# Performance work log

Measured on AMD Instinct MI355X. Metric: run time of the kernel, lower is better.

## Reference

```python
import jax, jax.numpy as jnp
import numpy as np


def setup_inputs() -> dict:
    key = jax.random.key(0)
    k1, k2, k3, k4, k5 = jax.random.split(key, 5)
    N, M, K = 200000, 50, 4
    T = 1000.0
    ti = jnp.sort(jax.random.uniform(k1, (N,), dtype=jnp.float32) * T)
    mi = jax.random.randint(k2, (N,), 0, M, dtype=jnp.int64)
    mu_at_events = jax.random.uniform(k3, (N,), dtype=jnp.float32) * 0.5 + 0.05
    alpha = jax.random.uniform(k4, (K, M, M), dtype=jnp.float32) * 0.1
    gamma = jax.random.uniform(k5, (K,), dtype=jnp.float32) * 2.0 + 0.5
    return {"ti": ti, "mi": mi, "mu_at_events": mu_at_events, "alpha": alpha, "gamma": gamma}


def _hawkes_logsum(ti, mi, mu_at_events, alpha, gamma):
    # ti: [N] sorted event times; mi: [N] event types in [0, M)
    # alpha: [K, M, M]; gamma: [K]; mu_at_events: [N]
    N = ti.shape[0]
    M = alpha.shape[1]
    # inter-event gaps; dt[0] = 0 so the first event has zero excitation state
    dt = jnp.concatenate([jnp.zeros((1,), ti.dtype), ti[1:] - ti[:-1]])  # [N]
    a = jnp.exp(-gamma[None, :] * dt[:, None])  # [N, K] decay factors
    # one-hot of the PREVIOUS event's type (row 0 is all-zero, matching e_mi)
    prev_onehot = jnp.zeros((N, M), ti.dtype).at[jnp.arange(1, N), mi[:-1]].set(1.0)
    b = a[:, None, :] * prev_onehot[:, :, None]  # [N, M, K]

    # linear recurrence S_i = a_i * S_{i-1} + b_i via associative scan
    # combine((a1,b1),(a2,b2)) = (a1*a2, a2*b1 + b2)
    def combine(x, y):
        a1, b1 = x
        a2, b2 = y
        return (a1 * a2, a2[:, None, :] * b1 + b2)

    _, S = jax.lax.associative_scan(combine, (a, b))  # S: [N, M, K]
    # S[i, m, k] = sum_{j < i, m_j = m} exp(-gamma_k (t_i - t_j))
    alpha_at = alpha[:, mi, :]  # [K, N, M] rows of alpha for each event's type
    lam = mu_at_events + jnp.einsum('knm,nmk,k->n', alpha_at, S, gamma)  # [N]
    return jnp.sum(jnp.log(lam))


def reference(ti, mi, mu_at_events, alpha, gamma):
    return _hawkes_logsum(ti, mi, mu_at_events, alpha, gamma)
```

## Files before the change

kernel.cpp:

```cpp
#include <hip/hip_runtime.h>
#include <hip/hip_bf16.h>

#define CHUNK 256
#define MM 50
#define KK 4
#define STATE (MM*KK)
#define ASTRIDE 51
#define SUP 32
#define NSMAX 26
#define NSUB 8
#define SUBSZ 32

__device__ __forceinline__ unsigned short f2bf(float x) {
  unsigned u = __float_as_uint(x);
  u += 0x7fffu + ((u >> 16) & 1u);
  return (unsigned short)(u >> 16);
}

__global__ __launch_bounds__(256) void phase1(
    const float* __restrict__ ti, const int* __restrict__ mi,
    const float* __restrict__ gamma, float* __restrict__ chunkB,
    float* __restrict__ superB, float* __restrict__ out0, int N, int G) {
  int g = blockIdx.x, tid = threadIdx.x;
  if (g == 0 && tid == 0) out0[0] = 0.f;
  int l = g * CHUNK;
  int r = min(N, l + CHUNK);
  __shared__ float Bs[STATE];
  __shared__ float g4[KK];
  if (tid < STATE) Bs[tid] = 0.f;
  if (tid < KK) g4[tid] = gamma[tid];
  __syncthreads();
  float t_end = ti[r - 1];
  int j0 = (g == 0) ? 0 : (l - 1);
  int j = j0 + tid;
  if (j <= r - 2) {
    int m = mi[j];
    float dt = t_end - ti[j];
    #pragma unroll
    for (int k = 0; k < KK; ++k)
      atomicAdd(&Bs[m * KK + k], __expf(-g4[k] * dt));
  }
  __syncthreads();
  if (tid < STATE) {
    float v = Bs[tid];
    chunkB[(size_t)g * STATE + tid] = v;
    int sup = g / SUP;
    float gk = g4[tid & 3];
    float Tsup = ti[min(N, (sup + 1) * SUP * CHUNK) - 1];
    atomicAdd(&superB[(size_t)sup * STATE + tid], __expf(-gk * (Tsup - t_end)) * v);
  }
}

__global__ __launch_bounds__(512) void phase3(
    const float* __restrict__ ti, const int* __restrict__ mi,
    const float* __restrict__ mu, const float* __restrict__ alpha,
    const float* __restrict__ gamma, const float* __restrict__ chunkB,
    const float* __restrict__ superB, float* __restrict__ out, int N, int G) {
  int g = blockIdx.x, tid = threadIdx.x;
  int l = g * CHUNK;
  int r = min(N, l + CHUNK);
  int cnt = r - l;
  int sup = g / SUP;
  int g0 = sup * SUP;
  int e = tid >> 1;
  int h = tid & 1;

  __shared__ unsigned P0[MM * ASTRIDE];
  __shared__ unsigned P1[MM * ASTRIDE];
  __shared__ __align__(16) float4 Fj[CHUNK];
  __shared__ int   cj[CHUNK];
  __shared__ __align__(16) float Q[NSUB][STATE];
  __shared__ float red8[8];
  __shared__ float teL[SUP];
  __shared__ float tlast[NSMAX];

  float gk0 = gamma[0], gk1 = gamma[1], gk2 = gamma[2], gk3 = gamma[3];

  for (int i = tid; i < NSUB * STATE; i += 512) ((float*)Q)[i] = 0.f;

  for (int idx = tid; idx < MM * MM; idx += 512) {
    int c = idx / MM, cp = idx - c * MM;
    float a0 = gk0 * alpha[idx];
    float a1 = gk1 * alpha[2500 + idx];
    float a2 = gk2 * alpha[5000 + idx];
    float a3 = gk3 * alpha[7500 + idx];
    P0[c * ASTRIDE + cp] = (unsigned)f2bf(a0) | ((unsigned)f2bf(a1) << 16);
    P1[c * ASTRIDE + cp] = (unsigned)f2bf(a2) | ((unsigned)f2bf(a3) << 16);
  }

  if (tid < SUP) {
    int c = g0 + tid;
    if (c < G) teL[tid] = ti[min(N, (c + 1) * CHUNK) - 1];
  } else if (tid >= 64 && tid < 64 + NSMAX) {
    int s = tid - 64;
    if (s < sup) tlast[s] = ti[min(N, (s + 1) * SUP * CHUNK) - 1];
  }

  float t_ref = ti[(g == 0) ? 0 : (l - 1)];
  if (tid < CHUNK) {
    int j = l - 1 + tid;
    bool valid = (j >= 0) && (j <= r - 2);
    float4 myF = make_float4(0.f, 0.f, 0.f, 0.f);
    int myc = 0;
    if (valid) {
      myc = mi[j];
      float tj = ti[j] - t_ref;
      myF = make_float4(__expf(gk0 * tj), __expf(gk1 * tj),
                        __expf(gk2 * tj), __expf(gk3 * tj));
    }
    cj[tid] = myc;
    Fj[tid] = myF;
    __syncthreads();
    if (valid) {
      float* q = &Q[tid >> 5][myc * KK];
      atomicAdd(q + 0, myF.x); atomicAdd(q + 1, myF.y);
      atomicAdd(q + 2, myF.z); atomicAdd(q + 3, myF.w);
    }
  } else {
    __syncthreads();
  }

  float S = 0.f;
  if (tid < STATE) {
    float gk = gamma[tid & 3];
    int nloc = g - g0;
    #pragma unroll 4
    for (int u = 0; u < nloc; ++u)
      S += __expf(-gk * (t_ref - teL[u])) * chunkB[(size_t)(g0 + u) * STATE + tid];
    #pragma unroll 4
    for (int s = 0; s < sup; ++s)
      S += __expf(-gk * (t_ref - tlast[s])) * superB[(size_t)s * STATE + tid];
  }
  __syncthreads();

  if (tid < STATE) {
    float run = S;
    #pragma unroll
    for (int q = 0; q < NSUB; ++q) {
      float t = Q[q][tid];
      Q[q][tid] = run;
      run += t;
    }
  }
  __syncthreads();

  float local = 0.f;
  {
    int c_n = (e < cnt) ? mi[l + e] : 0;
    int rowb = c_n * ASTRIDE;
    const float4* wb = (const float4*)&Q[e >> 5][0];
    float4 acc = make_float4(0.f, 0.f, 0.f, 0.f);
    if (e < cnt) {
      int mlo = h * 25, mhi = mlo + 25;
      #pragma unroll 5
      for (int m = mlo; m < mhi; ++m) {
        unsigned p0 = P0[rowb + m];
        unsigned p1 = P1[rowb + m];
        float4 w = wb[m];
        acc.x += __uint_as_float(p0 << 16)         * w.x;
        acc.y += __uint_as_float(p0 & 0xffff0000u) * w.y;
        acc.z += __uint_as_float(p1 << 16)         * w.z;
        acc.w += __uint_as_float(p1 & 0xffff0000u) * w.w;
      }
      #pragma unroll 4
      for (int s = (e & ~(SUBSZ - 1)) + h; s <= e; s += 2) {
        unsigned p0 = P0[rowb + cj[s]];
        unsigned p1 = P1[rowb + cj[s]];
        float4 f = Fj[s];
        acc.x += __uint_as_float(p0 << 16)         * f.x;
        acc.y += __uint_as_float(p0 & 0xffff0000u) * f.y;
        acc.z += __uint_as_float(p1 << 16)         * f.z;
        acc.w += __uint_as_float(p1 & 0xffff0000u) * f.w;
      }
    }
    acc.x += __shfl_xor(acc.x, 1, 64);
    acc.y += __shfl_xor(acc.y, 1, 64);
    acc.z += __shfl_xor(acc.z, 1, 64);
    acc.w += __shfl_xor(acc.w, 1, 64);
    if (h == 0 && e < cnt) {
      float tn = ti[l + e] - t_ref;
      float lam = mu[l + e]
                + __expf(-gk0 * tn) * acc.x + __expf(-gk1 * tn) * acc.y
                + __expf(-gk2 * tn) * acc.z + __expf(-gk3 * tn) * acc.w;
      local = __logf(lam);
    }
  }
  #pragma unroll
  for (int off = 32; off > 0; off >>= 1)
    local += __shfl_down(local, off, 64);
  if ((tid & 63) == 0) red8[tid >> 6] = local;
  __syncthreads();
  if (tid == 0) {
    float t = 0.f;
    #pragma unroll
    for (int w = 0; w < 8; ++w) t += red8[w];
    atomicAdd(out, t);
  }
}

extern "C" void kernel_launch(void* const* d_in, const int* in_sizes, int n_in,
                              void* d_out, int out_size, void* d_ws, size_t ws_size,
                              hipStream_t stream) {
  const float* ti    = (const float*)d_in[0];
  const int*   mi    = (const int*)d_in[1];
  const float* mu    = (const float*)d_in[2];
  const float* alpha = (const float*)d_in[3];
  const float* gamma = (const float*)d_in[4];
  float* out = (float*)d_out;
  int N = in_sizes[0];
  int G = (N + CHUNK - 1) / CHUNK;

  float* superB = (float*)d_ws;
  float* chunkB = superB + (size_t)NSMAX * STATE;

  phase1<<<G, 256, 0, stream>>>(ti, mi, gamma, chunkB, superB, out, N, G);
  phase3<<<G, 512, 0, stream>>>(ti, mi, mu, alpha, gamma, chunkB, superB, out, N, G);
}
```

Measured before the change: 89.60 us.

## Fuse both phases into one decoupled-lookback kernel with ticket-ordered chunks

Merges the chunk-summary pass and the evaluation pass into a single kernel. Each block takes a dynamic ticket for its chunk, computes its chunk summary from the already-built Q sums, and publishes it through flag variables in global memory. Later blocks spin-wait on earlier chunk flags and on superchunk flags before evaluating. This removes one kernel launch and the duplicate reads of ti and mi, at the cost of serialised spin-waits across blocks and a dependence on an epoch counter kept in persistent device globals.

Result: slower. 191.0 us (+113.2%).

```diff
diff --git a/kernel.cpp b/kernel.cpp
--- a/kernel.cpp
+++ b/kernel.cpp
@@ -1,5 +1,4 @@
 #include <hip/hip_runtime.h>
-#include <hip/hip_bf16.h>
 
 #define CHUNK 256
 #define MM 50
@@ -10,6 +9,13 @@
 #define NSMAX 26
 #define NSUB 8
 #define SUBSZ 32
+#define GMAX 1024
+
+__device__ int      g_ticket;
+__device__ unsigned g_flag[GMAX];
+__device__ unsigned g_sflag[64];
+__device__ float    g_chunkB[GMAX * STATE];
+__device__ float    g_superB[64 * STATE];
 
 __device__ __forceinline__ unsigned short f2bf(float x) {
   unsigned u = __float_as_uint(x);
@@ -17,54 +23,12 @@
   return (unsigned short)(u >> 16);
 }
 
-__global__ __launch_bounds__(256) void phase1(
-    const float* __restrict__ ti, const int* __restrict__ mi,
-    const float* __restrict__ gamma, float* __restrict__ chunkB,
-    float* __restrict__ superB, float* __restrict__ out0, int N, int G) {
-  int g = blockIdx.x, tid = threadIdx.x;
-  if (g == 0 && tid == 0) out0[0] = 0.f;
-  int l = g * CHUNK;
-  int r = min(N, l + CHUNK);
-  __shared__ float Bs[STATE];
-  __shared__ float g4[KK];
-  if (tid < STATE) Bs[tid] = 0.f;
-  if (tid < KK) g4[tid] = gamma[tid];
-  __syncthreads();
-  float t_end = ti[r - 1];
-  int j0 = (g == 0) ? 0 : (l - 1);
-  int j = j0 + tid;
-  if (j <= r - 2) {
-    int m = mi[j];
-    float dt = t_end - ti[j];
-    #pragma unroll
-    for (int k = 0; k < KK; ++k)
-      atomicAdd(&Bs[m * KK + k], __expf(-g4[k] * dt));
-  }
-  __syncthreads();
-  if (tid < STATE) {
-    float v = Bs[tid];
-    chunkB[(size_t)g * STATE + tid] = v;
-    int sup = g / SUP;
-    float gk = g4[tid & 3];
-    float Tsup = ti[min(N, (sup + 1) * SUP * CHUNK) - 1];
-    atomicAdd(&superB[(size_t)sup * STATE + tid], __expf(-gk * (Tsup - t_end)) * v);
-  }
-}
-
-__global__ __launch_bounds__(512) void phase3(
+__global__ __launch_bounds__(512) void hawkes_fused(
     const float* __restrict__ ti, const int* __restrict__ mi,
     const float* __restrict__ mu, const float* __restrict__ alpha,
-    const float* __restrict__ gamma, const float* __restrict__ chunkB,
-    const float* __restrict__ superB, float* __restrict__ out, int N, int G) {
-  int g = blockIdx.x, tid = threadIdx.x;
-  int l = g * CHUNK;
-  int r = min(N, l + CHUNK);
-  int cnt = r - l;
-  int sup = g / SUP;
-  int g0 = sup * SUP;
-  int e = tid >> 1;
-  int h = tid & 1;
-
+    const float* __restrict__ gamma, float* __restrict__ out, int N, int G) {
+  int tid = threadIdx.x;
+  __shared__ int vid_s;
   __shared__ unsigned P0[MM * ASTRIDE];
   __shared__ unsigned P1[MM * ASTRIDE];
   __shared__ __align__(16) float4 Fj[CHUNK];
@@ -74,6 +38,8 @@
   __shared__ float teL[SUP];
   __shared__ float tlast[NSMAX];
 
+  if (tid == 0) vid_s = atomicAdd(&g_ticket, 1);
+
   float gk0 = gamma[0], gk1 = gamma[1], gk2 = gamma[2], gk3 = gamma[3];
 
   for (int i = tid; i < NSUB * STATE; i += 512) ((float*)Q)[i] = 0.f;
@@ -87,6 +53,19 @@
     P0[c * ASTRIDE + cp] = (unsigned)f2bf(a0) | ((unsigned)f2bf(a1) << 16);
     P1[c * ASTRIDE + cp] = (unsigned)f2bf(a2) | ((unsigned)f2bf(a3) << 16);
   }
+  __syncthreads();
+
+  int tkt = vid_s;
+  int epoch = tkt / G;
+  int g = tkt - epoch * G;
+  unsigned DONE = (unsigned)epoch + 1u;
+  int l = g * CHUNK;
+  int r = min(N, l + CHUNK);
+  int cnt = r - l;
+  int sup = g / SUP;
+  int g0 = sup * SUP;
+  int e = tid >> 1;
+  int h = tid & 1;
 
   if (tid < SUP) {
     int c = g0 + tid;
@@ -97,11 +76,12 @@
   }
 
   float t_ref = ti[(g == 0) ? 0 : (l - 1)];
+  bool valid = false;
+  int myc = 0;
+  float4 myF = make_float4(0.f, 0.f, 0.f, 0.f);
   if (tid < CHUNK) {
     int j = l - 1 + tid;
-    bool valid = (j >= 0) && (j <= r - 2);
-    float4 myF = make_float4(0.f, 0.f, 0.f, 0.f);
-    int myc = 0;
+    valid = (j >= 0) && (j <= r - 2);
     if (valid) {
       myc = mi[j];
       float tj = ti[j] - t_ref;
@@ -110,36 +90,78 @@
     }
     cj[tid] = myc;
     Fj[tid] = myF;
-    __syncthreads();
-    if (valid) {
-      float* q = &Q[tid >> 5][myc * KK];
-      atomicAdd(q + 0, myF.x); atomicAdd(q + 1, myF.y);
-      atomicAdd(q + 2, myF.z); atomicAdd(q + 3, myF.w);
-    }
-  } else {
-    __syncthreads();
-  }
+  }
+  __syncthreads();
+
+  if (valid) {
+    float* q = &Q[tid >> 5][myc * KK];
+    atomicAdd(q + 0, myF.x); atomicAdd(q + 1, myF.y);
+    atomicAdd(q + 2, myF.z); atomicAdd(q + 3, myF.w);
+  }
+  __syncthreads();
+
+  float gk = (tid & 2) ? ((tid & 1) ? gk3 : gk2) : ((tid & 1) ? gk1 : gk0);
+  float Bv = 0.f, t_end = 0.f;
+  if (tid < STATE) {
+    t_end = teL[g - g0];
+    float tot = 0.f;
+    #pragma unroll
+    for (int q = 0; q < NSUB; ++q) tot += Q[q][tid];
+    Bv = __expf(-gk * (t_end - t_ref)) * tot;
+    g_chunkB[g * STATE + tid] = Bv;
+  }
+  if (g == 0 && tid == 0) out[0] = 0.f;
+  __syncthreads();
+  if (tid == 0) {
+    __builtin_amdgcn_fence(__ATOMIC_RELEASE, "agent");
+    __hip_atomic_store(&g_flag[g], DONE, __ATOMIC_RELAXED, __HIP_MEMORY_SCOPE_AGENT);
+  }
+
+  int nloc = g - g0;
+  if (tid < nloc) {
+    while (__hip_atomic_load(&g_flag[g0 + tid], __ATOMIC_RELAXED,
+                             __HIP_MEMORY_SCOPE_AGENT) != DONE)
+      __builtin_amdgcn_s_sleep(2);
+  }
+  __syncthreads();
+  __builtin_amdgcn_fence(__ATOMIC_ACQUIRE, "agent");
 
   float S = 0.f;
   if (tid < STATE) {
-    float gk = gamma[tid & 3];
-    int nloc = g - g0;
     #pragma unroll 4
     for (int u = 0; u < nloc; ++u)
-      S += __expf(-gk * (t_ref - teL[u])) * chunkB[(size_t)(g0 + u) * STATE + tid];
+      S += __expf(-gk * (t_ref - teL[u])) * g_chunkB[(g0 + u) * STATE + tid];
+  }
+
+  bool closer = (nloc == SUP - 1) || (g == G - 1);
+  if (closer) {
+    if (tid < STATE)
+      g_superB[sup * STATE + tid] = __expf(-gk * (t_end - t_ref)) * S + Bv;
+    __syncthreads();
+    if (tid == 0) {
+      __builtin_amdgcn_fence(__ATOMIC_RELEASE, "agent");
+      __hip_atomic_store(&g_sflag[sup], DONE, __ATOMIC_RELAXED, __HIP_MEMORY_SCOPE_AGENT);
+    }
+  }
+
+  if (tid < sup) {
+    while (__hip_atomic_load(&g_sflag[tid], __ATOMIC_RELAXED,
+                             __HIP_MEMORY_SCOPE_AGENT) != DONE)
+      __builtin_amdgcn_s_sleep(2);
+  }
+  __syncthreads();
+  __builtin_amdgcn_fence(__ATOMIC_ACQUIRE, "agent");
+
+  if (tid < STATE) {
     #pragma unroll 4
     for (int s = 0; s < sup; ++s)
-      S += __expf(-gk * (t_ref - tlast[s])) * superB[(size_t)s * STATE + tid];
-  }
-  __syncthreads();
-
-  if (tid < STATE) {
+      S += __expf(-gk * (t_ref - tlast[s])) * g_superB[s * STATE + tid];
     float run = S;
     #pragma unroll
     for (int q = 0; q < NSUB; ++q) {
-      float t = Q[q][tid];
+      float tq = Q[q][tid];
       Q[q][tid] = run;
-      run += t;
+      run += tq;
     }
   }
   __syncthreads();
@@ -191,10 +213,10 @@
   if ((tid & 63) == 0) red8[tid >> 6] = local;
   __syncthreads();
   if (tid == 0) {
-    float t = 0.f;
+    float acc8 = 0.f;
     #pragma unroll
-    for (int w = 0; w < 8; ++w) t += red8[w];
-    atomicAdd(out, t);
+    for (int w = 0; w < 8; ++w) acc8 += red8[w];
+    atomicAdd(out, acc8);
   }
 }
 
@@ -209,10 +231,7 @@
   float* out = (float*)d_out;
   int N = in_sizes[0];
   int G = (N + CHUNK - 1) / CHUNK;
-
-  float* superB = (float*)d_ws;
-  float* chunkB = superB + (size_t)NSMAX * STATE;
-
-  phase1<<<G, 256, 0, stream>>>(ti, mi, gamma, chunkB, superB, out, N, G);
-  phase3<<<G, 512, 0, stream>>>(ti, mi, mu, alpha, gamma, chunkB, superB, out, N, G);
+  if (G > GMAX) return;
+
+  hawkes_fused<<<G, 512, 0, stream>>>(ti, mi, mu, alpha, gamma, out, N, G);
 }
```
